# Kernel optimization log

Hardware: AMD Instinct MI355X
Metric: run time of the kernel (lower is better)

Reference implementation:

```python
import jax, jax.numpy as jnp
import numpy as np

_DN = ('NCHW', 'OIHW', 'NCHW')

def _conv(x, w, padding, groups=1):
    return jax.lax.conv_general_dilated(x, w, (1, 1), padding,
                                        dimension_numbers=_DN,
                                        feature_group_count=groups)

def _bn(x, g, b, m, v):  # eval-mode BatchNorm2d, eps=1e-5
    scale = (g * jax.lax.rsqrt(v + 1e-5))[None, :, None, None]
    return (x - m[None, :, None, None]) * scale + b[None, :, None, None]

def setup_inputs() -> dict:
    key = jax.random.key(0)
    ks = jax.random.split(key, 32)
    B, C, T = 128, 22, 1000
    sk = [1, 3, 5]
    tk = [64, 32, 16]
    inp = {}
    inp['x'] = jax.random.normal(ks[0], (B, 1, C, T), jnp.float32)
    for i, k in enumerate(sk):
        inp[f'ws{i}'] = jax.random.normal(ks[1 + i], (1, 1, k, 1), jnp.float32) * 0.3
    inp['bn_s_gamma'] = 1.0 + 0.1 * jax.random.normal(ks[4], (3,), jnp.float32)
    inp['bn_s_beta'] = 0.1 * jax.random.normal(ks[5], (3,), jnp.float32)
    inp['bn_s_mean'] = 0.1 * jax.random.normal(ks[6], (3,), jnp.float32)
    inp['bn_s_var'] = 0.5 + 0.5 * jax.random.uniform(ks[7], (3,), jnp.float32)
    total = sum(C - k + 1 for k in sk)  # 60
    inp['wf'] = jax.random.normal(ks[8], (50, 1, total, 1), jnp.float32) * 0.1
    inp['bn_f_gamma'] = 1.0 + 0.1 * jax.random.normal(ks[9], (50,), jnp.float32)
    inp['bn_f_beta'] = 0.1 * jax.random.normal(ks[10], (50,), jnp.float32)
    inp['bn_f_mean'] = 0.1 * jax.random.normal(ks[11], (50,), jnp.float32)
    inp['bn_f_var'] = 0.5 + 0.5 * jax.random.uniform(ks[12], (50,), jnp.float32)
    for i, k in enumerate(tk):
        inp[f'wt{i}'] = jax.random.normal(ks[13 + i], (150, 1, 1, k), jnp.float32) * 0.1
    inp['bn_t_gamma'] = 1.0 + 0.1 * jax.random.normal(ks[16], (3, 150), jnp.float32)
    inp['bn_t_beta'] = 0.1 * jax.random.normal(ks[17], (3, 150), jnp.float32)
    inp['bn_t_mean'] = 0.1 * jax.random.normal(ks[18], (3, 150), jnp.float32)
    inp['bn_t_var'] = 0.5 + 0.5 * jax.random.uniform(ks[19], (3, 150), jnp.float32)
    Q, _ = jnp.linalg.qr(jax.random.normal(ks[20], (450, 64), jnp.float32))
    inp['W_map'] = Q  # orthonormal columns, as in _initialize_bilinear
    inp['fc_w'] = jax.random.normal(ks[21], (4, 2080), jnp.float32) * 0.02
    inp['fc_b'] = jax.random.normal(ks[22], (4,), jnp.float32) * 0.02
    return inp

def reference(x, ws0, ws1, ws2, bn_s_gamma, bn_s_beta, bn_s_mean, bn_s_var,
              wf, bn_f_gamma, bn_f_beta, bn_f_mean, bn_f_var,
              wt0, wt1, wt2, bn_t_gamma, bn_t_beta, bn_t_mean, bn_t_var,
              W_map, fc_w, fc_b):
    B, T = x.shape[0], x.shape[3]  # time_length = 1000
    # --- spatial branches ---
    feats = []
    for i, w in enumerate((ws0, ws1, ws2)):
        o = _conv(x, w, 'VALID')  # [B,1,22-k+1,T]
        o = _bn(o, bn_s_gamma[i:i + 1], bn_s_beta[i:i + 1],
                bn_s_mean[i:i + 1], bn_s_var[i:i + 1])
        feats.append(o.reshape(B, 1, -1, T))
    xs = jnp.concatenate(feats, axis=2)  # [B,1,60,T]
    # --- spatial fusion ---
    xf = _bn(_conv(xs, wf, 'VALID'), bn_f_gamma, bn_f_beta, bn_f_mean, bn_f_var)  # [B,50,1,T]
    # --- temporal blocks (depthwise-expanded grouped convs) ---
    outs = []
    for i, w in enumerate((wt0, wt1, wt2)):
        k = w.shape[3]
        o = _conv(xf, w, [(0, 0), (k // 2, k // 2)], groups=xf.shape[1])  # [B,150,1,T+1]
        outs.append(_bn(o, bn_t_gamma[i], bn_t_beta[i], bn_t_mean[i], bn_t_var[i]))
    h = jnp.concatenate(outs, axis=1)[:, :, 0, :]  # [B,450,T+1]
    # --- covariance pooling + shrinkage ---
    cov = jnp.einsum('bct,bdt->bcd', h, h) / (T - 1)  # divide by time_length-1, as in source
    alpha = 0.05
    mu = jnp.mean(jnp.diagonal(cov, axis1=1, axis2=2), axis=1)  # [B]
    d = cov.shape[1]
    cov = (1.0 - alpha) * cov + alpha * mu[:, None, None] * jnp.eye(d, dtype=cov.dtype)
    # --- bilinear map + matrix log via eigh ---
    mapped = jnp.einsum('cm,bcd,dn->bmn', W_map, cov, W_map)  # [B,64,64]
    eigvals, eigvecs = jnp.linalg.eigh(mapped)
    log_eig = jnp.log(jnp.clip(eigvals, 1e-6))
    log_mapped = jnp.einsum('bim,bm,bjm->bij', eigvecs, log_eig, eigvecs)
    iu = jnp.triu_indices(mapped.shape[-1])
    features = log_mapped[:, iu[0], iu[1]]  # [B,2080]
    return features @ fc_w.T + fc_b  # [B,4]
```

## Files before the change

kernel.cpp:

```cpp
#include <hip/hip_runtime.h>
#include <math.h>


typedef __attribute__((ext_vector_type(4))) float v4f;

#define NSWEEP 6

#define WS_M      0
#define WS_BIASF  1100
#define WS_WTF    1152
#define WS_BT     17952
#define WS_HPART  18432
#define WS_Y      32768

__global__ void k_prep(
    const float* __restrict__ ws0, const float* __restrict__ ws1, const float* __restrict__ ws2,
    const float* __restrict__ bsg, const float* __restrict__ bsb, const float* __restrict__ bsm, const float* __restrict__ bsv,
    const float* __restrict__ wf,
    const float* __restrict__ bfg, const float* __restrict__ bfb, const float* __restrict__ bfm, const float* __restrict__ bfv,
    const float* __restrict__ wt0, const float* __restrict__ wt1, const float* __restrict__ wt2,
    const float* __restrict__ btg, const float* __restrict__ btb, const float* __restrict__ btm, const float* __restrict__ btv,
    float* __restrict__ wsf)
{
    int tid = threadIdx.x;
    if (tid < 450) {
        int c = tid;
        int i = c / 150, o = c % 150;
        int g = o / 3,   jr = o % 3;
        int k = (i == 0) ? 64 : ((i == 1) ? 32 : 16);
        float ga = btg[i*150 + o], bb = btb[i*150 + o];
        float mm = btm[i*150 + o], vv = btv[i*150 + o];
        float s = ga * rsqrtf(vv + 1e-5f);
        wsf[WS_BT + c] = bb - s * mm;
        int base = g*336 + ((i == 0) ? jr*64 : (i == 1) ? 192 + jr*32 : 288 + jr*16);
        const float* wsrc = (i == 0) ? wt0 : ((i == 1) ? wt1 : wt2);
        float* dst = wsf + WS_WTF + base;
        for (int t = 0; t < k; ++t) dst[t] = s * wsrc[o*k + t];
    }
    if (tid < 50) {
        int f = tid;
        float sf = bfg[f] * rsqrtf(bfv[f] + 1e-5f);
        float row[22];
        for (int c = 0; c < 22; ++c) row[c] = 0.f;
        float bacc = 0.f;
        for (int j = 0; j < 60; ++j) {
            int i, k, j0; const float* wsp;
            if (j < 22)      { i = 0; k = 1; j0 = j;      wsp = ws0; }
            else if (j < 42) { i = 1; k = 3; j0 = j - 22; wsp = ws1; }
            else             { i = 2; k = 5; j0 = j - 42; wsp = ws2; }
            float si = bsg[i] * rsqrtf(bsv[i] + 1e-5f);
            float bi = bsb[i] - si * bsm[i];
            float wfj = wf[f*60 + j];
            for (int d = 0; d < k; ++d) row[j0 + d] += wfj * si * wsp[d];
            bacc += wfj * bi;
        }
        for (int c = 0; c < 22; ++c) wsf[WS_M + f*22 + c] = sf * row[c];
        wsf[WS_BIASF + f] = sf * (bacc - bfm[f]) + bfb[f];
    }
}

__global__ __launch_bounds__(256) void k_main(
    const float* __restrict__ x, const float* __restrict__ wsf,
    const float* __restrict__ Wmap, float* __restrict__ y,
    float* __restrict__ hpart)
{
    const int b    = blockIdx.x >> 2;
    const int tile = blockIdx.x & 3;
    const int t0   = tile * 256;
    const int tid  = threadIdx.x;

    __shared__ float xt[25][320];
    __shared__ float wred[4];

    const float* Mg    = wsf + WS_M;
    const float* biasf = wsf + WS_BIASF;
    const float* wtf   = wsf + WS_WTF;
    const float* bt    = wsf + WS_BT;

    const int t = t0 + tid;
    const bool act = (t <= 1000);
    v4f yv4[16];
    #pragma unroll
    for (int m = 0; m < 16; ++m) yv4[m] = (v4f){0.f, 0.f, 0.f, 0.f};
    float hsq = 0.f;

    for (int ph = 0; ph < 2; ++ph) {
        const int gbase = 25 * ph;
        if (ph) __syncthreads();

        for (int col = tid; col < 320; col += 256) {
            int tx = t0 + col - 32;
            if (tx >= 0 && tx < 1000) {
                float xv[22];
                #pragma unroll
                for (int c = 0; c < 22; ++c) xv[c] = x[(b*22 + c)*1000 + tx];
                for (int gl = 0; gl < 25; ++gl) {
                    int g = gbase + gl;
                    float a = biasf[g];
                    #pragma unroll
                    for (int c = 0; c < 22; ++c) a += Mg[g*22 + c] * xv[c];
                    xt[gl][col] = a;
                }
            } else {
                for (int gl = 0; gl < 25; ++gl) xt[gl][col] = 0.f;
            }
        }
        __syncthreads();

        if (act) {
            for (int gl = 0; gl < 25; ++gl) {
                const int g = gbase + gl;
                const float* xb = &xt[gl][tid];
                const float* wg = wtf + g * 336;
                v4f h4[9];
                #pragma unroll
                for (int j = 0; j < 9; ++j) h4[j] = (v4f){0.f, 0.f, 0.f, 0.f};
                #pragma unroll
                for (int tau = 0; tau < 64; tau += 4) {
                    v4f xv = (v4f){xb[tau], xb[tau+1], xb[tau+2], xb[tau+3]};
                    h4[0] += (*(const v4f*)(wg + tau))       * xv;
                    h4[1] += (*(const v4f*)(wg + 64 + tau))  * xv;
                    h4[2] += (*(const v4f*)(wg + 128 + tau)) * xv;
                    if (tau >= 16 && tau < 48) {
                        int u = tau - 16;
                        h4[3] += (*(const v4f*)(wg + 192 + u)) * xv;
                        h4[4] += (*(const v4f*)(wg + 224 + u)) * xv;
                        h4[5] += (*(const v4f*)(wg + 256 + u)) * xv;
                    }
                    if (tau >= 24 && tau < 40) {
                        int u = tau - 24;
                        h4[6] += (*(const v4f*)(wg + 288 + u)) * xv;
                        h4[7] += (*(const v4f*)(wg + 304 + u)) * xv;
                        h4[8] += (*(const v4f*)(wg + 320 + u)) * xv;
                    }
                }
                #pragma unroll
                for (int j = 0; j < 9; ++j) {
                    int c = (j < 3) ? (3*g + j)
                          : (j < 6) ? (150 + 3*g + (j - 3))
                                    : (300 + 3*g + (j - 6));
                    float hv = (h4[j].x + h4[j].y) + (h4[j].z + h4[j].w) + bt[c];
                    hsq += hv * hv;
                    const v4f* wr4 = (const v4f*)(Wmap + c * 64);
                    v4f hv4 = (v4f){hv, hv, hv, hv};
                    #pragma unroll
                    for (int m = 0; m < 16; ++m) yv4[m] += wr4[m] * hv4;
                }
            }
        }
    }

    if (act) {
        #pragma unroll
        for (int k = 0; k < 16; ++k) {
            y[(b*64 + 4*k)*1001 + t]     = yv4[k].x;
            y[(b*64 + 4*k + 1)*1001 + t] = yv4[k].y;
            y[(b*64 + 4*k + 2)*1001 + t] = yv4[k].z;
            y[(b*64 + 4*k + 3)*1001 + t] = yv4[k].w;
        }
    }

    for (int off = 32; off > 0; off >>= 1) hsq += __shfl_down(hsq, off, 64);
    int wid = tid >> 6, lane = tid & 63;
    if (lane == 0) wred[wid] = hsq;
    __syncthreads();
    if (tid == 0) hpart[blockIdx.x] = wred[0] + wred[1] + wred[2] + wred[3];
}

__device__ __forceinline__ void pair_pq(int rr, int j, int& p, int& q) {
    if (j == 0) { p = 63; q = rr; }
    else {
        int a = rr + j;       if (a >= 63) a -= 63;
        int c = rr + 63 - j;  if (c >= 63) c -= 63;
        p = a; q = c;
    }
}

union SMu {
    float yt[64][129];
    struct { float A[64][65]; float V[64][65]; } j;
};

__global__ __launch_bounds__(1024) void k_eig(
    const float* __restrict__ y, const float* __restrict__ hpart,
    const float* __restrict__ fcw, const float* __restrict__ fcb,
    float* __restrict__ out)
{
    const int b    = blockIdx.x;
    const int tid  = threadIdx.x;
    const int w    = tid >> 6;
    const int lane = tid & 63;

    __shared__ SMu U;
    __shared__ float le[64];
    __shared__ float wred2[16];

    const int mg = tid >> 4, ng = tid & 15;
    const int m0 = mg * 4,  n0 = ng * 4;
    float acc[16];
    #pragma unroll
    for (int i = 0; i < 16; ++i) acc[i] = 0.f;
    for (int tile = 0; tile < 8; ++tile) {
        for (int idx = tid; idx < 64*128; idx += 1024) {
            int row = idx >> 7, col = idx & 127;
            int tg = tile * 128 + col;
            U.yt[row][col] = (tg <= 1000) ? y[(b*64 + row)*1001 + tg] : 0.f;
        }
        __syncthreads();
        if (tid < 256) {
            for (int tt = 0; tt < 128; ++tt) {
                float ym[4], yn[4];
                #pragma unroll
                for (int i = 0; i < 4; ++i) ym[i] = U.yt[m0 + i][tt];
                #pragma unroll
                for (int j = 0; j < 4; ++j) yn[j] = U.yt[n0 + j][tt];
                #pragma unroll
                for (int i = 0; i < 4; ++i)
                    #pragma unroll
                    for (int j = 0; j < 4; ++j) acc[i*4 + j] += ym[i] * yn[j];
            }
        }
        __syncthreads();
    }
    if (tid < 256) {
        float hs = hpart[b*4] + hpart[b*4+1] + hpart[b*4+2] + hpart[b*4+3];
        float mu = hs / (999.f * 450.f);
        #pragma unroll
        for (int i = 0; i < 4; ++i)
            #pragma unroll
            for (int j = 0; j < 4; ++j) {
                int mm = m0 + i, nn = n0 + j;
                U.j.A[mm][nn] = acc[i*4 + j] * (0.95f / 999.f)
                              + ((mm == nn) ? 0.05f * mu : 0.f);
                U.j.V[mm][nn] = (mm == nn) ? 1.f : 0.f;
            }
    }
    __syncthreads();

    for (int sweep = 0; sweep < NSWEEP; ++sweep)
    for (int rr = 0; rr < 63; ++rr) {
        float cp, sp;
        {
            int jj = w + ((lane & 1) << 4);
            int p, q; pair_pq(rr, jj, p, q);
            float app = U.j.A[p][p], aqq = U.j.A[q][q], apq = U.j.A[p][q];
            bool z = (fabsf(apq) <= 1e-30f);
            float apqs = z ? 1.f : apq;
            float tau = (aqq - app) * __builtin_amdgcn_rcpf(2.f * apqs);
            float tt = copysignf(1.f, tau) / (fabsf(tau) + sqrtf(1.f + tau*tau));
            float c = rsqrtf(1.f + tt*tt);
            float s = tt * c;
            cp = z ? 1.f : c;
            sp = z ? 0.f : s;
        }
        float c0 = __shfl(cp, 0, 64), s0 = __shfl(sp, 0, 64);
        float c1 = __shfl(cp, 1, 64), s1 = __shfl(sp, 1, 64);
        int p0, q0, p1, q1;
        pair_pq(rr, w,      p0, q0);
        pair_pq(rr, w + 16, p1, q1);

        float a0p = U.j.A[lane][p0], a0q = U.j.A[lane][q0];
        float a1p = U.j.A[lane][p1], a1q = U.j.A[lane][q1];
        float v0p = U.j.V[lane][p0], v0q = U.j.V[lane][q0];
        float v1p = U.j.V[lane][p1], v1q = U.j.V[lane][q1];
        U.j.A[lane][p0] = c0*a0p - s0*a0q;
        U.j.A[lane][q0] = s0*a0p + c0*a0q;
        U.j.A[lane][p1] = c1*a1p - s1*a1q;
        U.j.A[lane][q1] = s1*a1p + c1*a1q;
        U.j.V[lane][p0] = c0*v0p - s0*v0q;
        U.j.V[lane][q0] = s0*v0p + c0*v0q;
        U.j.V[lane][p1] = c1*v1p - s1*v1q;
        U.j.V[lane][q1] = s1*v1p + c1*v1q;
        __syncthreads();

        float r0p = U.j.A[p0][lane], r0q = U.j.A[q0][lane];
        float r1p = U.j.A[p1][lane], r1q = U.j.A[q1][lane];
        U.j.A[p0][lane] = c0*r0p - s0*r0q;
        U.j.A[q0][lane] = s0*r0p + c0*r0q;
        U.j.A[p1][lane] = c1*r1p - s1*r1q;
        U.j.A[q1][lane] = s1*r1p + c1*r1q;
        __syncthreads();
    }

    if (tid < 64) le[tid] = logf(fmaxf(U.j.A[tid][tid], 1e-6f));
    __syncthreads();

    if (tid < 256) {
        float lm[16];
        #pragma unroll
        for (int i = 0; i < 16; ++i) lm[i] = 0.f;
        for (int k = 0; k < 64; ++k) {
            float l = le[k];
            float vm[4], vn[4];
            #pragma unroll
            for (int i = 0; i < 4; ++i) vm[i] = U.j.V[m0 + i][k] * l;
            #pragma unroll
            for (int j = 0; j < 4; ++j) vn[j] = U.j.V[n0 + j][k];
            #pragma unroll
            for (int i = 0; i < 4; ++i)
                #pragma unroll
                for (int j = 0; j < 4; ++j) lm[i*4 + j] += vm[i] * vn[j];
        }

        float fa[4];
        #pragma unroll
        for (int o = 0; o < 4; ++o) fa[o] = 0.f;
        #pragma unroll
        for (int i = 0; i < 4; ++i)
            #pragma unroll
            for (int j = 0; j < 4; ++j) {
                int gi = m0 + i, gj = n0 + j;
                if (gi <= gj) {
                    int p = gi*64 - (gi*(gi-1))/2 + (gj - gi);
                    float lv = lm[i*4 + j];
                    #pragma unroll
                    for (int o = 0; o < 4; ++o) fa[o] += lv * fcw[o*2080 + p];
                }
            }

        #pragma unroll
        for (int o = 0; o < 4; ++o)
            for (int off = 32; off > 0; off >>= 1)
                fa[o] += __shfl_down(fa[o], off, 64);
        if (lane == 0) {
            #pragma unroll
            for (int o = 0; o < 4; ++o) wred2[w*4 + o] = fa[o];
        }
    }
    __syncthreads();
    if (tid < 4)
        out[b*4 + tid] = wred2[tid] + wred2[4 + tid] + wred2[8 + tid]
                       + wred2[12 + tid] + fcb[tid];
}

extern "C" void kernel_launch(void* const* d_in, const int* in_sizes, int n_in,
                              void* d_out, int out_size, void* d_ws, size_t ws_size,
                              hipStream_t stream) {
    (void)in_sizes; (void)n_in; (void)out_size; (void)ws_size;
    const float* x   = (const float*)d_in[0];
    const float* ws0 = (const float*)d_in[1];
    const float* ws1 = (const float*)d_in[2];
    const float* ws2 = (const float*)d_in[3];
    const float* bsg = (const float*)d_in[4];
    const float* bsb = (const float*)d_in[5];
    const float* bsm = (const float*)d_in[6];
    const float* bsv = (const float*)d_in[7];
    const float* wf  = (const float*)d_in[8];
    const float* bfg = (const float*)d_in[9];
    const float* bfb = (const float*)d_in[10];
    const float* bfm = (const float*)d_in[11];
    const float* bfv = (const float*)d_in[12];
    const float* wt0 = (const float*)d_in[13];
    const float* wt1 = (const float*)d_in[14];
    const float* wt2 = (const float*)d_in[15];
    const float* btg = (const float*)d_in[16];
    const float* btb = (const float*)d_in[17];
    const float* btm = (const float*)d_in[18];
    const float* btv = (const float*)d_in[19];
    const float* Wm  = (const float*)d_in[20];
    const float* fcw = (const float*)d_in[21];
    const float* fcb = (const float*)d_in[22];

    float* wsf   = (float*)d_ws;
    float* yb    = wsf + WS_Y;
    float* hpart = wsf + WS_HPART;

    k_prep<<<1, 512, 0, stream>>>(ws0, ws1, ws2, bsg, bsb, bsm, bsv,
                                  wf, bfg, bfb, bfm, bfv,
                                  wt0, wt1, wt2, btg, btb, btm, btv, wsf);
    k_main<<<512, 256, 0, stream>>>(x, wsf, Wm, yb, hpart);
    k_eig<<<128, 1024, 0, stream>>>(yb, hpart, fcw, fcb, (float*)d_out);
}
```

Baseline: 735.5 us.

## Halve k_eig block size and give each wave four Jacobi rotation pairs

Changes the eigen kernel from 1024 to 512 threads per block, so 8 waves each apply four Jacobi rotation pairs per round instead of 16 waves doing two each. The goal is cheaper __syncthreads barriers across fewer waves and more independent LDS work per wave in the serial sweep loop. The tradeoff is less parallelism in the covariance-tile load and in the other phases. Those phases gated on tid<256 are unaffected.

Result: slower. 772.2 us (+5.0%).

```diff
diff --git a/kernel.cpp b/kernel.cpp
--- a/kernel.cpp
+++ b/kernel.cpp
@@ -181,7 +181,7 @@
     struct { float A[64][65]; float V[64][65]; } j;
 };
 
-__global__ __launch_bounds__(1024) void k_eig(
+__global__ __launch_bounds__(512) void k_eig(
     const float* __restrict__ y, const float* __restrict__ hpart,
     const float* __restrict__ fcw, const float* __restrict__ fcb,
     float* __restrict__ out)
@@ -201,7 +201,7 @@
     #pragma unroll
     for (int i = 0; i < 16; ++i) acc[i] = 0.f;
     for (int tile = 0; tile < 8; ++tile) {
-        for (int idx = tid; idx < 64*128; idx += 1024) {
+        for (int idx = tid; idx < 64*128; idx += 512) {
             int row = idx >> 7, col = idx & 127;
             int tg = tile * 128 + col;
             U.yt[row][col] = (tg <= 1000) ? y[(b*64 + row)*1001 + tg] : 0.f;
@@ -241,7 +241,7 @@
     for (int rr = 0; rr < 63; ++rr) {
         float cp, sp;
         {
-            int jj = w + ((lane & 1) << 4);
+            int jj = w + ((lane & 3) << 3);
             int p, q; pair_pq(rr, jj, p, q);
             float app = U.j.A[p][p], aqq = U.j.A[q][q], apq = U.j.A[p][q];
             bool z = (fabsf(apq) <= 1e-30f);
@@ -253,32 +253,45 @@
             cp = z ? 1.f : c;
             sp = z ? 0.f : s;
         }
-        float c0 = __shfl(cp, 0, 64), s0 = __shfl(sp, 0, 64);
-        float c1 = __shfl(cp, 1, 64), s1 = __shfl(sp, 1, 64);
-        int p0, q0, p1, q1;
-        pair_pq(rr, w,      p0, q0);
-        pair_pq(rr, w + 16, p1, q1);
-
-        float a0p = U.j.A[lane][p0], a0q = U.j.A[lane][q0];
-        float a1p = U.j.A[lane][p1], a1q = U.j.A[lane][q1];
-        float v0p = U.j.V[lane][p0], v0q = U.j.V[lane][q0];
-        float v1p = U.j.V[lane][p1], v1q = U.j.V[lane][q1];
-        U.j.A[lane][p0] = c0*a0p - s0*a0q;
-        U.j.A[lane][q0] = s0*a0p + c0*a0q;
-        U.j.A[lane][p1] = c1*a1p - s1*a1q;
-        U.j.A[lane][q1] = s1*a1p + c1*a1q;
-        U.j.V[lane][p0] = c0*v0p - s0*v0q;
-        U.j.V[lane][q0] = s0*v0p + c0*v0q;
-        U.j.V[lane][p1] = c1*v1p - s1*v1q;
-        U.j.V[lane][q1] = s1*v1p + c1*v1q;
-        __syncthreads();
-
-        float r0p = U.j.A[p0][lane], r0q = U.j.A[q0][lane];
-        float r1p = U.j.A[p1][lane], r1q = U.j.A[q1][lane];
-        U.j.A[p0][lane] = c0*r0p - s0*r0q;
-        U.j.A[q0][lane] = s0*r0p + c0*r0q;
-        U.j.A[p1][lane] = c1*r1p - s1*r1q;
-        U.j.A[q1][lane] = s1*r1p + c1*r1q;
+        float cr[4], sr[4];
+        int pA[4], qA[4];
+        #pragma unroll
+        for (int k = 0; k < 4; ++k) {
+            cr[k] = __shfl(cp, k, 64);
+            sr[k] = __shfl(sp, k, 64);
+            pair_pq(rr, w + 8*k, pA[k], qA[k]);
+        }
+
+        float ap[4], aq[4], vp[4], vq[4];
+        #pragma unroll
+        for (int k = 0; k < 4; ++k) {
+            ap[k] = U.j.A[lane][pA[k]];
+            aq[k] = U.j.A[lane][qA[k]];
+            vp[k] = U.j.V[lane][pA[k]];
+            vq[k] = U.j.V[lane][qA[k]];
+        }
+        #pragma unroll
+        for (int k = 0; k < 4; ++k) {
+            float c = cr[k], s = sr[k];
+            U.j.A[lane][pA[k]] = c*ap[k] - s*aq[k];
+            U.j.A[lane][qA[k]] = s*ap[k] + c*aq[k];
+            U.j.V[lane][pA[k]] = c*vp[k] - s*vq[k];
+            U.j.V[lane][qA[k]] = s*vp[k] + c*vq[k];
+        }
+        __syncthreads();
+
+        float rp[4], rq[4];
+        #pragma unroll
+        for (int k = 0; k < 4; ++k) {
+            rp[k] = U.j.A[pA[k]][lane];
+            rq[k] = U.j.A[qA[k]][lane];
+        }
+        #pragma unroll
+        for (int k = 0; k < 4; ++k) {
+            float c = cr[k], s = sr[k];
+            U.j.A[pA[k]][lane] = c*rp[k] - s*rq[k];
+            U.j.A[qA[k]][lane] = s*rp[k] + c*rq[k];
+        }
         __syncthreads();
     }
 
@@ -369,5 +382,5 @@
                                   wf, bfg, bfb, bfm, bfv,
                                   wt0, wt1, wt2, btg, btb, btm, btv, wsf);
     k_main<<<512, 256, 0, stream>>>(x, wsf, Wm, yb, hpart);
-    k_eig<<<128, 1024, 0, stream>>>(yb, hpart, fcw, fcb, (float*)d_out);
-}
+    k_eig<<<128, 512, 0, stream>>>(yb, hpart, fcw, fcb, (float*)d_out);
+}
```
